# Kernel optimization log

Hardware: AMD Instinct MI355X
Metric: run time of the kernel (lower is better)

## Reference

```python
import jax, jax.numpy as jnp
import numpy as np

B, NV, H, D = 8, 16, 192, 512
NH = 8
HD = D // NH
DFF = 2048
EPS = 1e-5


def _bn(x, g, b):
    # x: (N, T, C); BatchNorm1d over channel C using batch stats (train mode)
    mu = jnp.mean(x, axis=(0, 1))
    var = jnp.var(x, axis=(0, 1))
    return (x - mu) / jnp.sqrt(var + EPS) * g + b


def _ff(x, w1, b1, w2, b2):
    h = jax.nn.gelu(jnp.einsum('bnhd,fd->bnhf', x, w1) + b1, approximate=False)
    return jnp.einsum('bnhf,df->bnhd', h, w2) + b2


def setup_inputs() -> dict:
    key = jax.random.key(0)
    ks = jax.random.split(key, 20)
    s = 0.02
    return {
        'src': jax.random.normal(ks[0], (B, NV, H, D), jnp.float32),
        'qk_w': jax.random.normal(ks[1], (2 * D, D), jnp.float32) * s,
        'qk_b': jnp.zeros((2 * D,), jnp.float32),
        'v_w': jax.random.normal(ks[2], (D, D), jnp.float32) * s,
        'v_b': jnp.zeros((D,), jnp.float32),
        'alpha_p': jax.random.normal(ks[3], (HD, 1), jnp.float32) * 0.1,
        'g_pre1': jnp.ones((D,), jnp.float32),
        'b_pre1': jnp.zeros((D,), jnp.float32),
        'g_pre2': jnp.ones((D,), jnp.float32),
        'b_pre2': jnp.zeros((D,), jnp.float32),
        'ff1_w1': jax.random.normal(ks[4], (DFF, D), jnp.float32) * s,
        'ff1_b1': jnp.zeros((DFF,), jnp.float32),
        'ff1_w2': jax.random.normal(ks[5], (D, DFF), jnp.float32) * s,
        'ff1_b2': jnp.zeros((D,), jnp.float32),
        'ff2_w1': jax.random.normal(ks[6], (DFF, D), jnp.float32) * s,
        'ff2_b1': jnp.zeros((DFF,), jnp.float32),
        'ff2_w2': jax.random.normal(ks[7], (D, DFF), jnp.float32) * s,
        'ff2_b2': jnp.zeros((D,), jnp.float32),
        'g_attn': jnp.ones((D,), jnp.float32),
        'b_attn': jnp.zeros((D,), jnp.float32),
    }


def reference(src, qk_w, qk_b, v_w, v_b, alpha_p,
              g_pre1, b_pre1, g_pre2, b_pre2,
              ff1_w1, ff1_b1, ff1_w2, ff1_b2,
              ff2_w1, ff2_b1, ff2_w2, ff2_b2,
              g_attn, b_attn):
    b, n, h, c = src.shape
    hd = c // NH
    # normalized input for q,k; raw for v
    src1 = src / jnp.linalg.norm(src, axis=-1, keepdims=True)
    qk = (jnp.einsum('bnhc,ec->bnhe', src1, qk_w) + qk_b)
    qk = qk.reshape(b, n, h, 2, NH, hd).transpose(3, 0, 1, 4, 2, 5)  # (2,b,n,NH,h,hd)
    q, k = qk[0], qk[1]
    v = (jnp.einsum('bnhc,ec->bnhe', src, v_w) + v_b)
    v = v.reshape(b, n, h, NH, hd).transpose(0, 1, 3, 2, 4)  # (b,n,NH,h,hd)

    # exponential-decay weights in FFT domain (branch: h != 7)
    a = jax.nn.sigmoid(alpha_p)                  # (hd,1)
    ar = jnp.arange(h - 1, -1, -1, dtype=src.dtype)
    weights = a * (1.0 - a) ** ar                # (hd, h)
    n2 = 2 * h
    w_f = jnp.fft.rfft(weights, n=n2, axis=-1)   # (hd, h+1)
    q_f = jnp.swapaxes(jnp.fft.rfft(q, n=n2, axis=-2), -1, -2) * w_f
    k_f = jnp.swapaxes(jnp.fft.rfft(k, n=n2, axis=-2), -1, -2) * w_f
    q1 = jnp.swapaxes(jnp.fft.irfft(q_f, n=n2, axis=-1)[..., :h], -1, -2)
    k1 = jnp.swapaxes(jnp.fft.irfft(k_f, n=n2, axis=-1)[..., :h], -1, -2)

    # token-axis attention (note: original divides by head_dim**-0.5 == * sqrt(hd))
    score_t = jnp.einsum('bnhed,bnhfd->bnhef', q1, k1) * (hd ** 0.5)
    attn_t = jax.nn.softmax(score_t, axis=-1)
    out_tok = jnp.einsum('bnhef,bnhfd->bnhed', attn_t, v)  # (b,n,NH,h,hd)
    o3 = _bn(out_tok.reshape(b * n, h, NH * hd), g_pre2, b_pre2).reshape(b, n, h, c)

    # hidden-axis attention on un-decayed q,k (scale = sqrt(h))
    score_h = jnp.einsum('bnhae,bnhaf->bnhef', q, k) * (h ** 0.5)
    attn_h = jax.nn.softmax(score_h, axis=-1)
    out_hid = jnp.einsum('bnhef,bnhaf->bnhae', attn_h, v)  # (b,n,NH,h,hd)
    o2 = _bn(out_hid.reshape(b * n, h, NH * hd), g_pre1, b_pre1).reshape(b, n, h, c)

    src2 = _ff(o3, ff1_w1, ff1_b1, ff1_w2, ff1_b2) + _ff(o2, ff2_w1, ff2_b1, ff2_w2, ff2_b2)
    out = src + src2
    out = _bn(out.reshape(b * n, h, c), g_attn, b_attn).reshape(b, n, h, c)
    return out
```

## Files before the change

kernel.cpp:

```cpp
#include <hip/hip_runtime.h>
#include <math.h>

#define SEQ 192
#define NTOK 24576
#define EPS 1e-5f

typedef __bf16 bf16x8 __attribute__((ext_vector_type(8)));
typedef __bf16 bf16x4 __attribute__((ext_vector_type(4)));
typedef float  f32x4  __attribute__((ext_vector_type(4)));

__device__ __forceinline__ void load_lds16(const __bf16* g, __bf16* l) {
    __builtin_amdgcn_global_load_lds(
        (const __attribute__((address_space(1))) uint32_t*)g,
        (__attribute__((address_space(3))) uint32_t*)l, 16, 0, 0);
}

__device__ __forceinline__ float gelu_f(float x) {
    float z = 1.5957691216057308f * x * fmaf(0.044715f, x*x, 1.f);
    float e = __expf(-z);
    return x * __builtin_amdgcn_rcpf(1.f + e);
}

__global__ __launch_bounds__(256) void cvtall_k(
    const float* __restrict__ s0, const float* __restrict__ s1, const float* __restrict__ s2,
    const float* __restrict__ s3, const float* __restrict__ s4, const float* __restrict__ s5,
    __bf16* __restrict__ dst)
{
    int i = blockIdx.x * 256 + threadIdx.x;
    int f = i * 4;
    const float* s; int off;
    if      (f <  524288) { s = s0; off = 0;       }
    else if (f <  786432) { s = s1; off = 524288;  }
    else if (f < 1835008) { s = s2; off = 786432;  }
    else if (f < 2883584) { s = s3; off = 1835008; }
    else if (f < 3932160) { s = s4; off = 2883584; }
    else                  { s = s5; off = 3932160; }
    f32x4 v = *(const f32x4*)&s[f - off];
    bf16x4 o;
    o[0]=(__bf16)v[0]; o[1]=(__bf16)v[1]; o[2]=(__bf16)v[2]; o[3]=(__bf16)v[3];
    ((bf16x4*)dst)[i] = o;
}

__global__ __launch_bounds__(256) void prep_k(const float* __restrict__ src,
    __bf16* __restrict__ srcb, __bf16* __restrict__ srcnb)
{
    int w = threadIdx.x >> 6, lane = threadIdx.x & 63;
    size_t token = blockIdx.x * 4 + w;
    const float* p = src + token * 512 + lane * 8;
    f32x4 a0 = *(const f32x4*)p;
    f32x4 a1 = *(const f32x4*)(p + 4);
    float s = a0[0]*a0[0]+a0[1]*a0[1]+a0[2]*a0[2]+a0[3]*a0[3]
            + a1[0]*a1[0]+a1[1]*a1[1]+a1[2]*a1[2]+a1[3]*a1[3];
#pragma unroll
    for (int off = 32; off; off >>= 1) s += __shfl_xor(s, off);
    float rs = rsqrtf(s);
    bf16x8 vb, vn;
#pragma unroll
    for (int q = 0; q < 4; q++) {
        vb[q]   = (__bf16)a0[q];      vn[q]   = (__bf16)(a0[q]*rs);
        vb[q+4] = (__bf16)a1[q];      vn[q+4] = (__bf16)(a1[q]*rs);
    }
    *(bf16x8*)&srcb[token*512 + lane*8]  = vb;
    *(bf16x8*)&srcnb[token*512 + lane*8] = vn;
}

template<bool AFFINE, bool GELU>
__global__ __launch_bounds__(256) void gemm_k(
    const __bf16* __restrict__ A, const __bf16* __restrict__ B, __bf16* __restrict__ C,
    int N, int K, const float* __restrict__ bias, const float* __restrict__ coef)
{
    __shared__ __bf16 As[8192];
    __shared__ __bf16 Bs[8192];
    const int tid = threadIdx.x, lane = tid & 63, w = tid >> 6;
    const int wr = w >> 1, wc = w & 1;
    const int b = blockIdx.y * gridDim.x + blockIdx.x;
    const int xcd = b & 7, bi = b >> 3;
    const int ypx = gridDim.y >> 3;
    const int m0 = (xcd * ypx + bi / gridDim.x) * 128;
    const int n0 = (bi % gridDim.x) * 128;
    const int fr = lane & 15, fq = lane >> 4;
    const int grow = 8*w + (lane >> 3);
    const int gcol = ((lane & 7) ^ (lane >> 3)) * 8;
    const __bf16* gB = B + (size_t)(n0 + grow) * K + gcol;
    const __bf16* gA = A + (size_t)(m0 + grow) * K + gcol;
    __bf16* ldsA = As + 8*w*64 + lane*8;
    __bf16* ldsB = Bs + 8*w*64 + lane*8;

    f32x4 acc[4][4];
#pragma unroll
    for (int i = 0; i < 4; i++)
#pragma unroll
        for (int j = 0; j < 4; j++) acc[i][j] = (f32x4){0.f,0.f,0.f,0.f};

    for (int k0 = 0; k0 < K; k0 += 64) {
        if (!AFFINE) {
#pragma unroll
            for (int i = 0; i < 4; i++)
                load_lds16(gA + k0 + (size_t)(32*i)*K, ldsA + i*2048);
        } else {
            const int r = tid >> 3, cseg = tid & 7;
            const float* scp = coef + k0 + cseg*8;
            const float* shp = coef + 512 + k0 + cseg*8;
            f32x4 sc0 = *(const f32x4*)scp, sc1 = *(const f32x4*)(scp+4);
            f32x4 sh0 = *(const f32x4*)shp, sh1 = *(const f32x4*)(shp+4);
#pragma unroll
            for (int i = 0; i < 4; i++) {
                int row = 32*i + r;
                bf16x8 a = *(const bf16x8*)&A[(size_t)(m0+row)*512 + k0 + cseg*8];
                bf16x8 v;
#pragma unroll
                for (int q = 0; q < 4; q++) {
                    v[q]   = (__bf16)fmaf((float)a[q],   sc0[q], sh0[q]);
                    v[q+4] = (__bf16)fmaf((float)a[q+4], sc1[q], sh1[q]);
                }
                *(bf16x8*)&As[row*64 + ((cseg ^ (r & 7)) * 8)] = v;
            }
        }
#pragma unroll
        for (int i = 0; i < 4; i++)
            load_lds16(gB + k0 + (size_t)(32*i)*K, ldsB + i*2048);
        __syncthreads();
#pragma unroll
        for (int kk = 0; kk < 2; kk++) {
            bf16x8 af[4], bfv[4];
#pragma unroll
            for (int i = 0; i < 4; i++)
                af[i] = *(bf16x8*)&As[(wr*64 + i*16 + fr)*64 + (((kk*4+fq) ^ (fr&7))*8)];
#pragma unroll
            for (int j = 0; j < 4; j++)
                bfv[j] = *(bf16x8*)&Bs[(wc*64 + j*16 + fr)*64 + (((kk*4+fq) ^ (fr&7))*8)];
#pragma unroll
            for (int i = 0; i < 4; i++)
#pragma unroll
                for (int j = 0; j < 4; j++)
                    acc[i][j] = __builtin_amdgcn_mfma_f32_16x16x32_bf16(af[i], bfv[j], acc[i][j], 0, 0, 0);
        }
        __syncthreads();
    }
    const int r4 = lane >> 4, cc = lane & 15;
#pragma unroll
    for (int i = 0; i < 4; i++) {
#pragma unroll
        for (int r = 0; r < 4; r++) {
            int m = m0 + wr*64 + i*16 + r4*4 + r;
#pragma unroll
            for (int j = 0; j < 4; j++) {
                int n = n0 + wc*64 + j*16 + cc;
                float v = acc[i][j][r] + bias[n];
                if (GELU) v = gelu_f(v);
                C[(size_t)m * N + n] = (__bf16)v;
            }
        }
    }
}

__global__ __launch_bounds__(256) void w1scale_k(
    __bf16* __restrict__ w, const float* __restrict__ coef,
    const float* __restrict__ bias_in, float* __restrict__ bias_out)
{
    const int wv = threadIdx.x >> 6, lane = threadIdx.x & 63;
    const int n = blockIdx.x * 4 + wv;
    __bf16* p = w + (size_t)n * 512 + lane * 8;
    bf16x8 v = *(bf16x8*)p;
    f32x4 sc0 = *(const f32x4*)(coef + lane*8);
    f32x4 sc1 = *(const f32x4*)(coef + lane*8 + 4);
    f32x4 sh0 = *(const f32x4*)(coef + 512 + lane*8);
    f32x4 sh1 = *(const f32x4*)(coef + 512 + lane*8 + 4);
    float dot = 0.f;
    bf16x8 o;
#pragma unroll
    for (int q = 0; q < 4; q++) {
        float w0 = (float)v[q], w1 = (float)v[q+4];
        o[q]   = (__bf16)(w0 * sc0[q]);
        o[q+4] = (__bf16)(w1 * sc1[q]);
        dot = fmaf(w0, sh0[q], dot);
        dot = fmaf(w1, sh1[q], dot);
    }
    *(bf16x8*)p = o;
#pragma unroll
    for (int off = 32; off; off >>= 1) dot += __shfl_xor(dot, off);
    if (lane == 0) bias_out[n] = bias_in[n] + dot;
}

__global__ __launch_bounds__(256) void gemm2_k(
    const __bf16* __restrict__ A1, const __bf16* __restrict__ A2,
    const __bf16* __restrict__ B1, const __bf16* __restrict__ B2,
    float* __restrict__ C, const float* __restrict__ b1, const float* __restrict__ b2,
    const float* __restrict__ resid, float* __restrict__ st)
{
    __shared__ __bf16 As[4096];
    __shared__ __bf16 Bs[8192];
    const int tid = threadIdx.x, lane = tid & 63, w = tid >> 6;
    const int wr = w >> 1, wc = w & 1;
    const int vb = blockIdx.x;
    const int xcd = vb & 7, k2 = vb >> 3;
    const int m0 = (xcd*24 + (k2 >> 2)) * 64;
    const int n0 = (k2 & 3) * 128;
    const int fr = lane & 15, fq = lane >> 4;
    const int grow = 8*w + (lane >> 3);
    const int gcol = ((lane & 7) ^ (lane >> 3)) * 8;
    const int K = 2048;
    __bf16* ldsA = As + 8*w*64 + lane*8;
    __bf16* ldsB = Bs + 8*w*64 + lane*8;

    f32x4 acc[2][4];
#pragma unroll
    for (int i = 0; i < 2; i++)
#pragma unroll
        for (int j = 0; j < 4; j++) acc[i][j] = (f32x4){0.f,0.f,0.f,0.f};

#pragma unroll 1
    for (int half = 0; half < 2; half++) {
        const __bf16* gA = (half ? A2 : A1) + (size_t)(m0 + grow) * K + gcol;
        const __bf16* gB = (half ? B2 : B1) + (size_t)(n0 + grow) * K + gcol;
        for (int k0 = 0; k0 < K; k0 += 64) {
            load_lds16(gA + k0,                 ldsA);
            load_lds16(gA + k0 + (size_t)32*K,  ldsA + 2048);
#pragma unroll
            for (int i = 0; i < 4; i++)
                load_lds16(gB + k0 + (size_t)(32*i)*K, ldsB + i*2048);
            __syncthreads();
#pragma unroll
            for (int kk = 0; kk < 2; kk++) {
                bf16x8 af[2], bfv[4];
#pragma unroll
                for (int i = 0; i < 2; i++)
                    af[i] = *(bf16x8*)&As[(wr*32 + i*16 + fr)*64 + (((kk*4+fq) ^ (fr&7))*8)];
#pragma unroll
                for (int j = 0; j < 4; j++)
                    bfv[j] = *(bf16x8*)&Bs[(wc*64 + j*16 + fr)*64 + (((kk*4+fq) ^ (fr&7))*8)];
#pragma unroll
                for (int i = 0; i < 2; i++)
#pragma unroll
                    for (int j = 0; j < 4; j++)
                        acc[i][j] = __builtin_amdgcn_mfma_f32_16x16x32_bf16(af[i], bfv[j], acc[i][j], 0, 0, 0);
            }
            __syncthreads();
        }
    }
    const int r4 = lane >> 4, cc = lane & 15;
    float cs[4] = {0,0,0,0}, cq[4] = {0,0,0,0};
#pragma unroll
    for (int i = 0; i < 2; i++) {
#pragma unroll
        for (int r = 0; r < 4; r++) {
            int m = m0 + wr*32 + i*16 + r4*4 + r;
#pragma unroll
            for (int j = 0; j < 4; j++) {
                int n = n0 + wc*64 + j*16 + cc;
                size_t idx = (size_t)m * 512 + n;
                float v = acc[i][j][r] + b1[n] + b2[n] + resid[idx];
                C[idx] = v;
                cs[j] += v; cq[j] = fmaf(v, v, cq[j]);
            }
        }
    }
#pragma unroll
    for (int j = 0; j < 4; j++) {
        cs[j] += __shfl_xor(cs[j], 16); cs[j] += __shfl_xor(cs[j], 32);
        cq[j] += __shfl_xor(cq[j], 16); cq[j] += __shfl_xor(cq[j], 32);
    }
    if (r4 == 0) {
#pragma unroll
        for (int j = 0; j < 4; j++) {
            int n = n0 + wc*64 + j*16 + cc;
            atomicAdd(&st[n], cs[j]);
            atomicAdd(&st[512 + n], cq[j]);
        }
    }
}

__global__ __launch_bounds__(256) void hidden_attn_mfma_k(
    const __bf16* __restrict__ QKb, const __bf16* __restrict__ Vb, __bf16* __restrict__ OHb)
{
    __shared__ __bf16 smem[25600];
    __bf16* Qt = smem;
    __bf16* Kt = smem + 12800;
    __bf16* Ps = smem;
    __bf16* Vs = smem + 4608;
    const int bn = blockIdx.x >> 3, nh = blockIdx.x & 7;
    const int tid = threadIdx.x, lane = tid & 63, w = tid >> 6;
    const int fr = lane & 15, fq = lane >> 4;
    const size_t rowbase = (size_t)bn * SEQ;

#pragma unroll
    for (int it = 0; it < 12; it++) {
        int tk = tid + (it % 6) * 256;
        int j = tk & 63, tg = tk >> 6;
        const __bf16* gsrc = QKb + (rowbase + tg*8)*1024 + nh*64 + j + (it >= 6 ? 512 : 0);
        bf16x8 v;
#pragma unroll
        for (int u = 0; u < 8; u++) v[u] = gsrc[(size_t)u*1024];
        __bf16* dst = (it >= 6 ? Kt : Qt) + j*200 + tg*8;
        *(bf16x8*)dst = v;
    }
    __syncthreads();

    f32x4 acc[4];
#pragma unroll
    for (int i = 0; i < 4; i++) acc[i] = (f32x4){0.f,0.f,0.f,0.f};
#pragma unroll
    for (int kc = 0; kc < 6; kc++) {
        bf16x8 a = *(bf16x8*)&Qt[(w*16 + fr)*200 + kc*32 + fq*8];
#pragma unroll
        for (int nt = 0; nt < 4; nt++) {
            bf16x8 b = *(bf16x8*)&Kt[(nt*16 + fr)*200 + kc*32 + fq*8];
            acc[nt] = __builtin_amdgcn_mfma_f32_16x16x32_bf16(a, b, acc[nt], 0, 0, 0);
        }
    }
    const float sc = 13.856406460551018f;
    float pn[4][4];
#pragma unroll
    for (int reg = 0; reg < 4; reg++) {
        float m = -1e30f;
#pragma unroll
        for (int nt = 0; nt < 4; nt++) { acc[nt][reg] *= sc; m = fmaxf(m, acc[nt][reg]); }
#pragma unroll
        for (int off = 1; off < 16; off <<= 1) m = fmaxf(m, __shfl_xor(m, off));
        float l = 0.f;
#pragma unroll
        for (int nt = 0; nt < 4; nt++) { pn[nt][reg] = __expf(acc[nt][reg] - m); l += pn[nt][reg]; }
#pragma unroll
        for (int off = 1; off < 16; off <<= 1) l += __shfl_xor(l, off);
        float inv = 1.f / l;
#pragma unroll
        for (int nt = 0; nt < 4; nt++) pn[nt][reg] *= inv;
    }
    __syncthreads();
#pragma unroll
    for (int nt = 0; nt < 4; nt++)
#pragma unroll
        for (int reg = 0; reg < 4; reg++)
            Ps[(w*16 + fq*4 + reg)*72 + nt*16 + fr] = (__bf16)pn[nt][reg];
    for (int i = tid; i < 1536; i += 256) {
        int t = i >> 3, s = i & 7;
        *(bf16x8*)&Vs[t*72 + s*8] = *(const bf16x8*)&Vb[(rowbase+t)*512 + nh*64 + s*8];
    }
    __syncthreads();

    f32x4 o[3][4];
#pragma unroll
    for (int i = 0; i < 3; i++)
#pragma unroll
        for (int j = 0; j < 4; j++) o[i][j] = (f32x4){0.f,0.f,0.f,0.f};
#pragma unroll
    for (int kc = 0; kc < 2; kc++) {
        bf16x8 av[3];
#pragma unroll
        for (int mt = 0; mt < 3; mt++)
            av[mt] = *(bf16x8*)&Vs[(48*w + mt*16 + fr)*72 + kc*32 + fq*8];
#pragma unroll
        for (int nt = 0; nt < 4; nt++) {
            bf16x8 b = *(bf16x8*)&Ps[(nt*16 + fr)*72 + kc*32 + fq*8];
#pragma unroll
            for (int mt = 0; mt < 3; mt++)
                o[mt][nt] = __builtin_amdgcn_mfma_f32_16x16x32_bf16(av[mt], b, o[mt][nt], 0, 0, 0);
        }
    }
    __bf16* obase = OHb + ((size_t)(bn*8 + nh)) * SEQ * 64;
#pragma unroll
    for (int mt = 0; mt < 3; mt++)
#pragma unroll
        for (int reg = 0; reg < 4; reg++) {
            int t = 48*w + mt*16 + fq*4 + reg;
#pragma unroll
            for (int nt = 0; nt < 4; nt++)
                obase[(size_t)t*64 + nt*16 + fr] = (__bf16)o[mt][nt][reg];
        }
}

__global__ __launch_bounds__(256) void token_attn_mfma_k(
    const __bf16* __restrict__ QKb, const __bf16* __restrict__ Vb, __bf16* __restrict__ OT,
    const float* __restrict__ alpha)
{
    __shared__ __bf16 smem[27648];
    __bf16* Qs = smem;
    __bf16* Ks = smem + 13824;
    __bf16* Vt = smem;
    __bf16* Pw = smem + 12800;
    const int bn = blockIdx.x >> 3, nh = blockIdx.x & 7;
    const int tid = threadIdx.x, lane = tid & 63, w = tid >> 6;
    const int fr = lane & 15, fq = lane >> 4;
    const size_t rowbase = (size_t)bn * SEQ;

    for (int i = tid; i < 1536; i += 256) {
        int t = i >> 3, s = i & 7;
        const __bf16* g = QKb + (rowbase + t)*1024 + nh*64;
        *(bf16x8*)&Qs[t*72 + s*8] = *(const bf16x8*)&g[s*8];
        *(bf16x8*)&Ks[t*72 + s*8] = *(const bf16x8*)&g[512 + s*8];
    }
    __syncthreads();

    if (tid < 128) {
        const int d = tid & 63;
        __bf16* col = (tid < 64) ? (Qs + d) : (Ks + d);
        const float av = 1.f / (1.f + __expf(-alpha[d]));
        const float r = 1.f - av;
        float P = 0.f, pw = 1.f;
#pragma unroll 4
        for (int t = 0; t < SEQ; t++) {
            P = fmaf(pw, (float)col[t*72], P);
            col[t*72] = (__bf16)P;
            pw *= r;
        }
        float f = av;
#pragma unroll 4
        for (int t = SEQ-1; t >= 0; t--) {
            col[t*72] = (__bf16)((float)col[t*72] * f);
            f *= r;
        }
    }
    __syncthreads();

    f32x4 S[3][12];
#pragma unroll
    for (int i = 0; i < 3; i++)
#pragma unroll
        for (int j = 0; j < 12; j++) S[i][j] = (f32x4){0.f,0.f,0.f,0.f};
#pragma unroll
    for (int kc = 0; kc < 2; kc++) {
        bf16x8 aq[3];
#pragma unroll
        for (int mt = 0; mt < 3; mt++)
            aq[mt] = *(bf16x8*)&Qs[(48*w + mt*16 + fr)*72 + kc*32 + fq*8];
#pragma unroll
        for (int nt = 0; nt < 12; nt++) {
            bf16x8 b = *(bf16x8*)&Ks[(nt*16 + fr)*72 + kc*32 + fq*8];
#pragma unroll
            for (int mt = 0; mt < 3; mt++)
                S[mt][nt] = __builtin_amdgcn_mfma_f32_16x16x32_bf16(aq[mt], b, S[mt][nt], 0, 0, 0);
        }
    }
#pragma unroll
    for (int mt = 0; mt < 3; mt++)
#pragma unroll
        for (int reg = 0; reg < 4; reg++) {
            float m = -1e30f;
#pragma unroll
            for (int nt = 0; nt < 12; nt++) { S[mt][nt][reg] *= 8.f; m = fmaxf(m, S[mt][nt][reg]); }
#pragma unroll
            for (int off = 1; off < 16; off <<= 1) m = fmaxf(m, __shfl_xor(m, off));
            float l = 0.f;
#pragma unroll
            for (int nt = 0; nt < 12; nt++) { S[mt][nt][reg] = __expf(S[mt][nt][reg] - m); l += S[mt][nt][reg]; }
#pragma unroll
            for (int off = 1; off < 16; off <<= 1) l += __shfl_xor(l, off);
            float inv = 1.f / l;
#pragma unroll
            for (int nt = 0; nt < 12; nt++) S[mt][nt][reg] *= inv;
        }
    __syncthreads();
#pragma unroll
    for (int it = 0; it < 6; it++) {
        int tk = tid + it * 256;
        int d = tk & 63, tg = tk >> 6;
        const __bf16* gsrc = Vb + (rowbase + tg*8)*512 + nh*64 + d;
        bf16x8 v;
#pragma unroll
        for (int u = 0; u < 8; u++) v[u] = gsrc[(size_t)u*512];
        *(bf16x8*)&Vt[d*200 + tg*8] = v;
    }
    __syncthreads();

    f32x4 O[3][4];
#pragma unroll
    for (int i = 0; i < 3; i++)
#pragma unroll
        for (int j = 0; j < 4; j++) O[i][j] = (f32x4){0.f,0.f,0.f,0.f};
    __bf16* myP = Pw + w*3456;
#pragma unroll
    for (int fc = 0; fc < 3; fc++) {
#pragma unroll
        for (int mt = 0; mt < 3; mt++)
#pragma unroll
            for (int j = 0; j < 4; j++)
#pragma unroll
                for (int reg = 0; reg < 4; reg++)
                    myP[(mt*16 + fq*4 + reg)*72 + j*16 + fr] = (__bf16)S[mt][fc*4 + j][reg];
#pragma unroll
        for (int kc = 0; kc < 2; kc++) {
            bf16x8 ap[3];
#pragma unroll
            for (int mt = 0; mt < 3; mt++)
                ap[mt] = *(bf16x8*)&myP[(mt*16 + fr)*72 + kc*32 + fq*8];
#pragma unroll
            for (int dt = 0; dt < 4; dt++) {
                bf16x8 b = *(bf16x8*)&Vt[(dt*16 + fr)*200 + fc*64 + kc*32 + fq*8];
#pragma unroll
                for (int mt = 0; mt < 3; mt++)
                    O[mt][dt] = __builtin_amdgcn_mfma_f32_16x16x32_bf16(ap[mt], b, O[mt][dt], 0, 0, 0);
            }
        }
    }
    __bf16* obase = OT + ((size_t)(bn*8 + nh)) * SEQ * 64;
#pragma unroll
    for (int mt = 0; mt < 3; mt++)
#pragma unroll
        for (int reg = 0; reg < 4; reg++) {
            int e = 48*w + mt*16 + fq*4 + reg;
#pragma unroll
            for (int dt = 0; dt < 4; dt++)
                obase[(size_t)e*64 + dt*16 + fr] = (__bf16)O[mt][dt][reg];
        }
}

__global__ __launch_bounds__(256) void bn_stats1_k(const __bf16* __restrict__ x, float* __restrict__ part)
{
    __shared__ float red[3072];
    const int col8 = threadIdx.x & 63;
    const int rl   = threadIdx.x >> 6;
    const size_t r0 = (size_t)blockIdx.x * 96;
    f32x4 sA = {0,0,0,0}, sB = {0,0,0,0}, qA = {0,0,0,0}, qB = {0,0,0,0};
    for (int r = rl; r < 96; r += 4) {
        bf16x8 v = *(const bf16x8*)&x[(r0 + r)*512 + col8*8];
        f32x4 lo = { (float)v[0], (float)v[1], (float)v[2], (float)v[3] };
        f32x4 hi = { (float)v[4], (float)v[5], (float)v[6], (float)v[7] };
        sA += lo; sB += hi;
        qA += lo*lo; qB += hi*hi;
    }
    if (rl > 0) {
        float* p = &red[(rl-1)*1024];
        *(f32x4*)&p[col8*8]       = sA;  *(f32x4*)&p[col8*8 + 4]       = sB;
        *(f32x4*)&p[512 + col8*8] = qA;  *(f32x4*)&p[512 + col8*8 + 4] = qB;
    }
    __syncthreads();
    if (rl == 0) {
#pragma unroll
        for (int k = 0; k < 3; k++) {
            float* p = &red[k*1024];
            sA += *(f32x4*)&p[col8*8];       sB += *(f32x4*)&p[col8*8 + 4];
            qA += *(f32x4*)&p[512 + col8*8]; qB += *(f32x4*)&p[512 + col8*8 + 4];
        }
        float* o = &part[(size_t)blockIdx.x * 1024];
        *(f32x4*)&o[col8*8]       = sA;  *(f32x4*)&o[col8*8 + 4]       = sB;
        *(f32x4*)&o[512 + col8*8] = qA;  *(f32x4*)&o[512 + col8*8 + 4] = qB;
    }
}

__global__ __launch_bounds__(256) void bn_stats2_k(const float* __restrict__ part, float* __restrict__ st)
{
    int c = blockIdx.x * 256 + threadIdx.x;
    float s0 = 0.f, s1 = 0.f, s2 = 0.f, s3 = 0.f;
    for (int b = 0; b < 256; b += 4) {
        s0 += part[(size_t)b*1024 + c];
        s1 += part[(size_t)(b+1)*1024 + c];
        s2 += part[(size_t)(b+2)*1024 + c];
        s3 += part[(size_t)(b+3)*1024 + c];
    }
    st[c] = (s0 + s1) + (s2 + s3);
}

__global__ void bn_coef_k(const float* __restrict__ st, const float* __restrict__ g,
                          const float* __restrict__ b, float* __restrict__ coef)
{
    int c = threadIdx.x;
    float mean = st[c] * (1.f/24576.f);
    float var  = st[512+c] * (1.f/24576.f) - mean*mean;
    float sc = rsqrtf(var + EPS) * g[c];
    coef[c] = sc;
    coef[512 + c] = b[c] - mean * sc;
}

__global__ __launch_bounds__(256) void bn_apply4_k(const float* __restrict__ x, const float* __restrict__ st,
    const float* __restrict__ g, const float* __restrict__ b, float* __restrict__ out)
{
    size_t i = (size_t)blockIdx.x * 256 + threadIdx.x;
    int col4 = i & 127;
    f32x4 v = ((const f32x4*)x)[i];
    f32x4 sm = ((const f32x4*)st)[col4];
    f32x4 sq = ((const f32x4*)(st + 512))[col4];
    f32x4 o;
#pragma unroll
    for (int j = 0; j < 4; j++) {
        int c = col4*4 + j;
        float mean = sm[j] * (1.f/24576.f);
        float var  = sq[j] * (1.f/24576.f) - mean*mean;
        o[j] = (v[j] - mean) * rsqrtf(var + EPS) * g[c] + b[c];
    }
    ((f32x4*)out)[i] = o;
}

extern "C" void kernel_launch(void* const* d_in, const int* in_sizes, int n_in,
                              void* d_out, int out_size, void* d_ws, size_t ws_size,
                              hipStream_t stream)
{
    const float* src    = (const float*)d_in[0];
    const float* qk_w   = (const float*)d_in[1];
    const float* qk_b   = (const float*)d_in[2];
    const float* v_w    = (const float*)d_in[3];
    const float* v_b    = (const float*)d_in[4];
    const float* alpha  = (const float*)d_in[5];
    const float* g_pre1 = (const float*)d_in[6];
    const float* b_pre1 = (const float*)d_in[7];
    const float* g_pre2 = (const float*)d_in[8];
    const float* b_pre2 = (const float*)d_in[9];
    const float* ff1_w1 = (const float*)d_in[10];
    const float* ff1_b1 = (const float*)d_in[11];
    const float* ff1_w2 = (const float*)d_in[12];
    const float* ff1_b2 = (const float*)d_in[13];
    const float* ff2_w1 = (const float*)d_in[14];
    const float* ff2_b1 = (const float*)d_in[15];
    const float* ff2_w2 = (const float*)d_in[16];
    const float* ff2_b2 = (const float*)d_in[17];
    const float* g_attn = (const float*)d_in[18];
    const float* b_attn = (const float*)d_in[19];
    float* out = (float*)d_out;

    __bf16* wq   = (__bf16*)d_ws;
    __bf16* wv   = wq  + 524288;
    __bf16* w11  = wv  + 262144;
    __bf16* w12  = w11 + 1048576;
    __bf16* w21  = w12 + 1048576;
    __bf16* w22  = w21 + 1048576;
    __bf16* srcb  = w22 + 1048576;
    __bf16* srcnb = srcb + (size_t)NTOK*512;
    __bf16* QKb   = srcnb + (size_t)NTOK*512;
    __bf16* Vb    = QKb + (size_t)NTOK*1024;
    __bf16* OHbf  = Vb + (size_t)NTOK*512;
    __bf16* o3bf  = OHbf + (size_t)NTOK*512;
    float*  stats = (float*)(o3bf + (size_t)NTOK*512);
    float*  coef0 = stats + 3072;
    float*  coef1 = coef0 + 1024;
    float*  part0 = coef1 + 1024;
    float*  part1 = part0 + 262144;
    float*  bias1p = part1 + 262144;
    float*  bias2p = bias1p + 2048;
    __bf16* H1 = srcb;
    __bf16* H2 = H1 + (size_t)12288*2048;
    float *st0 = stats, *st1 = stats + 1024, *st2 = stats + 2048;

    hipMemsetAsync(st2, 0, 1024*sizeof(float), stream);

    cvtall_k<<<4864, 256, 0, stream>>>(qk_w, v_w, ff1_w1, ff1_w2, ff2_w1, ff2_w2, wq);
    prep_k<<<NTOK/4, 256, 0, stream>>>(src, srcb, srcnb);

    gemm_k<false,false><<<dim3(8, 192), 256, 0, stream>>>(srcnb, wq, QKb, 1024, 512, qk_b, nullptr);
    gemm_k<false,false><<<dim3(4, 192), 256, 0, stream>>>(srcb,  wv, Vb,  512,  512, v_b,  nullptr);

    hidden_attn_mfma_k<<<1024, 256, 0, stream>>>(QKb, Vb, OHbf);

    token_attn_mfma_k<<<1024, 256, 0, stream>>>(QKb, Vb, o3bf, alpha);

    bn_stats1_k<<<256, 256, 0, stream>>>(o3bf, part0);
    bn_stats1_k<<<256, 256, 0, stream>>>(OHbf, part1);
    bn_stats2_k<<<4, 256, 0, stream>>>(part0, st0);
    bn_stats2_k<<<4, 256, 0, stream>>>(part1, st1);
    bn_coef_k<<<1, 512, 0, stream>>>(st0, g_pre2, b_pre2, coef0);
    bn_coef_k<<<1, 512, 0, stream>>>(st1, g_pre1, b_pre1, coef1);
    w1scale_k<<<512, 256, 0, stream>>>(w11, coef0, ff1_b1, bias1p);
    w1scale_k<<<512, 256, 0, stream>>>(w21, coef1, ff2_b1, bias2p);

    for (int ch = 0; ch < 2; ch++) {
        size_t off = (size_t)ch * 12288 * 512;
        gemm_k<false,true><<<dim3(16, 96), 256, 0, stream>>>(o3bf + off, w11, H1, 2048, 512, bias1p, nullptr);
        gemm_k<false,true><<<dim3(16, 96), 256, 0, stream>>>(OHbf + off, w21, H2, 2048, 512, bias2p, nullptr);
        gemm2_k<<<768, 256, 0, stream>>>(H1, H2, w12, w22, out + off,
                                         ff1_b2, ff2_b2, src + off, st2);
    }

    bn_apply4_k<<<12288, 256, 0, stream>>>(out, st2, g_attn, b_attn, out);
}
```

Before: 696.9 us.

## Merge small launches, fuse attention kernels, double-buffer the second FFN GEMM

Several pairs of kernels become single launches: weight conversion with input prep, the two attention kernels (interleaved by block parity), the BN stat and coefficient kernels, the W1 scaling, and the two first-layer FFN GEMMs, which now share one grid through a DUAL path. The unused AFFINE path is removed from the GEMM. The second FFN GEMM now double-buffers its LDS tiles, prefetching the next K slice while computing the current one, with one barrier per iteration. The aim is to cut launch overhead and tail idle time and to hide global-load latency, at the cost of twice the LDS in gemm2, which may reduce occupancy.

Result: no change. 695.5 us (-0.2%).

```diff
diff --git a/kernel.cpp b/kernel.cpp
--- a/kernel.cpp
+++ b/kernel.cpp
@@ -21,53 +21,55 @@
     return x * __builtin_amdgcn_rcpf(1.f + e);
 }
 
-__global__ __launch_bounds__(256) void cvtall_k(
+__global__ __launch_bounds__(256) void cvtprep_k(
     const float* __restrict__ s0, const float* __restrict__ s1, const float* __restrict__ s2,
     const float* __restrict__ s3, const float* __restrict__ s4, const float* __restrict__ s5,
-    __bf16* __restrict__ dst)
-{
-    int i = blockIdx.x * 256 + threadIdx.x;
-    int f = i * 4;
-    const float* s; int off;
-    if      (f <  524288) { s = s0; off = 0;       }
-    else if (f <  786432) { s = s1; off = 524288;  }
-    else if (f < 1835008) { s = s2; off = 786432;  }
-    else if (f < 2883584) { s = s3; off = 1835008; }
-    else if (f < 3932160) { s = s4; off = 2883584; }
-    else                  { s = s5; off = 3932160; }
-    f32x4 v = *(const f32x4*)&s[f - off];
-    bf16x4 o;
-    o[0]=(__bf16)v[0]; o[1]=(__bf16)v[1]; o[2]=(__bf16)v[2]; o[3]=(__bf16)v[3];
-    ((bf16x4*)dst)[i] = o;
-}
-
-__global__ __launch_bounds__(256) void prep_k(const float* __restrict__ src,
-    __bf16* __restrict__ srcb, __bf16* __restrict__ srcnb)
-{
-    int w = threadIdx.x >> 6, lane = threadIdx.x & 63;
-    size_t token = blockIdx.x * 4 + w;
-    const float* p = src + token * 512 + lane * 8;
-    f32x4 a0 = *(const f32x4*)p;
-    f32x4 a1 = *(const f32x4*)(p + 4);
-    float s = a0[0]*a0[0]+a0[1]*a0[1]+a0[2]*a0[2]+a0[3]*a0[3]
-            + a1[0]*a1[0]+a1[1]*a1[1]+a1[2]*a1[2]+a1[3]*a1[3];
-#pragma unroll
-    for (int off = 32; off; off >>= 1) s += __shfl_xor(s, off);
-    float rs = rsqrtf(s);
-    bf16x8 vb, vn;
-#pragma unroll
-    for (int q = 0; q < 4; q++) {
-        vb[q]   = (__bf16)a0[q];      vn[q]   = (__bf16)(a0[q]*rs);
-        vb[q+4] = (__bf16)a1[q];      vn[q+4] = (__bf16)(a1[q]*rs);
-    }
-    *(bf16x8*)&srcb[token*512 + lane*8]  = vb;
-    *(bf16x8*)&srcnb[token*512 + lane*8] = vn;
-}
-
-template<bool AFFINE, bool GELU>
+    __bf16* __restrict__ dst,
+    const float* __restrict__ src, __bf16* __restrict__ srcb, __bf16* __restrict__ srcnb)
+{
+    if (blockIdx.x < 4864) {
+        int i = blockIdx.x * 256 + threadIdx.x;
+        int f = i * 4;
+        const float* s; int off;
+        if      (f <  524288) { s = s0; off = 0;       }
+        else if (f <  786432) { s = s1; off = 524288;  }
+        else if (f < 1835008) { s = s2; off = 786432;  }
+        else if (f < 2883584) { s = s3; off = 1835008; }
+        else if (f < 3932160) { s = s4; off = 2883584; }
+        else                  { s = s5; off = 3932160; }
+        f32x4 v = *(const f32x4*)&s[f - off];
+        bf16x4 o;
+        o[0]=(__bf16)v[0]; o[1]=(__bf16)v[1]; o[2]=(__bf16)v[2]; o[3]=(__bf16)v[3];
+        ((bf16x4*)dst)[i] = o;
+    } else {
+        int blk = blockIdx.x - 4864;
+        int w = threadIdx.x >> 6, lane = threadIdx.x & 63;
+        size_t token = blk * 4 + w;
+        const float* p = src + token * 512 + lane * 8;
+        f32x4 a0 = *(const f32x4*)p;
+        f32x4 a1 = *(const f32x4*)(p + 4);
+        float s = a0[0]*a0[0]+a0[1]*a0[1]+a0[2]*a0[2]+a0[3]*a0[3]
+                + a1[0]*a1[0]+a1[1]*a1[1]+a1[2]*a1[2]+a1[3]*a1[3];
+#pragma unroll
+        for (int off = 32; off; off >>= 1) s += __shfl_xor(s, off);
+        float rs = rsqrtf(s);
+        bf16x8 vb, vn;
+#pragma unroll
+        for (int q = 0; q < 4; q++) {
+            vb[q]   = (__bf16)a0[q];      vn[q]   = (__bf16)(a0[q]*rs);
+            vb[q+4] = (__bf16)a1[q];      vn[q+4] = (__bf16)(a1[q]*rs);
+        }
+        *(bf16x8*)&srcb[token*512 + lane*8]  = vb;
+        *(bf16x8*)&srcnb[token*512 + lane*8] = vn;
+    }
+}
+
+template<bool GELU, bool DUAL>
 __global__ __launch_bounds__(256) void gemm_k(
     const __bf16* __restrict__ A, const __bf16* __restrict__ B, __bf16* __restrict__ C,
-    int N, int K, const float* __restrict__ bias, const float* __restrict__ coef)
+    int N, int K, const float* __restrict__ bias,
+    const __bf16* __restrict__ A2, const __bf16* __restrict__ B2, __bf16* __restrict__ C2,
+    const float* __restrict__ bias2, int M1)
 {
     __shared__ __bf16 As[8192];
     __shared__ __bf16 Bs[8192];
@@ -76,8 +78,9 @@
     const int b = blockIdx.y * gridDim.x + blockIdx.x;
     const int xcd = b & 7, bi = b >> 3;
     const int ypx = gridDim.y >> 3;
-    const int m0 = (xcd * ypx + bi / gridDim.x) * 128;
+    int m0 = (xcd * ypx + bi / gridDim.x) * 128;
     const int n0 = (bi % gridDim.x) * 128;
+    if (DUAL && m0 >= M1) { A = A2; B = B2; C = C2; bias = bias2; m0 -= M1; }
     const int fr = lane & 15, fq = lane >> 4;
     const int grow = 8*w + (lane >> 3);
     const int gcol = ((lane & 7) ^ (lane >> 3)) * 8;
@@ -93,29 +96,9 @@
         for (int j = 0; j < 4; j++) acc[i][j] = (f32x4){0.f,0.f,0.f,0.f};
 
     for (int k0 = 0; k0 < K; k0 += 64) {
-        if (!AFFINE) {
-#pragma unroll
-            for (int i = 0; i < 4; i++)
-                load_lds16(gA + k0 + (size_t)(32*i)*K, ldsA + i*2048);
-        } else {
-            const int r = tid >> 3, cseg = tid & 7;
-            const float* scp = coef + k0 + cseg*8;
-            const float* shp = coef + 512 + k0 + cseg*8;
-            f32x4 sc0 = *(const f32x4*)scp, sc1 = *(const f32x4*)(scp+4);
-            f32x4 sh0 = *(const f32x4*)shp, sh1 = *(const f32x4*)(shp+4);
-#pragma unroll
-            for (int i = 0; i < 4; i++) {
-                int row = 32*i + r;
-                bf16x8 a = *(const bf16x8*)&A[(size_t)(m0+row)*512 + k0 + cseg*8];
-                bf16x8 v;
-#pragma unroll
-                for (int q = 0; q < 4; q++) {
-                    v[q]   = (__bf16)fmaf((float)a[q],   sc0[q], sh0[q]);
-                    v[q+4] = (__bf16)fmaf((float)a[q+4], sc1[q], sh1[q]);
-                }
-                *(bf16x8*)&As[row*64 + ((cseg ^ (r & 7)) * 8)] = v;
-            }
-        }
+#pragma unroll
+        for (int i = 0; i < 4; i++)
+            load_lds16(gA + k0 + (size_t)(32*i)*K, ldsA + i*2048);
 #pragma unroll
         for (int i = 0; i < 4; i++)
             load_lds16(gB + k0 + (size_t)(32*i)*K, ldsB + i*2048);
@@ -155,12 +138,18 @@
 }
 
 __global__ __launch_bounds__(256) void w1scale_k(
-    __bf16* __restrict__ w, const float* __restrict__ coef,
-    const float* __restrict__ bias_in, float* __restrict__ bias_out)
-{
+    __bf16* __restrict__ w1a, __bf16* __restrict__ w1b, const float* __restrict__ coef01,
+    const float* __restrict__ b1in, const float* __restrict__ b2in,
+    float* __restrict__ b1out, float* __restrict__ b2out)
+{
+    const int half = blockIdx.x >> 9;
+    __bf16* wbase = half ? w1b : w1a;
+    const float* coef = coef01 + half*1024;
+    const float* bin  = half ? b2in  : b1in;
+    float* bout       = half ? b2out : b1out;
     const int wv = threadIdx.x >> 6, lane = threadIdx.x & 63;
-    const int n = blockIdx.x * 4 + wv;
-    __bf16* p = w + (size_t)n * 512 + lane * 8;
+    const int n = (blockIdx.x & 511) * 4 + wv;
+    __bf16* p = wbase + (size_t)n * 512 + lane * 8;
     bf16x8 v = *(bf16x8*)p;
     f32x4 sc0 = *(const f32x4*)(coef + lane*8);
     f32x4 sc1 = *(const f32x4*)(coef + lane*8 + 4);
@@ -179,7 +168,7 @@
     *(bf16x8*)p = o;
 #pragma unroll
     for (int off = 32; off; off >>= 1) dot += __shfl_xor(dot, off);
-    if (lane == 0) bias_out[n] = bias_in[n] + dot;
+    if (lane == 0) bout[n] = bin[n] + dot;
 }
 
 __global__ __launch_bounds__(256) void gemm2_k(
@@ -188,8 +177,8 @@
     float* __restrict__ C, const float* __restrict__ b1, const float* __restrict__ b2,
     const float* __restrict__ resid, float* __restrict__ st)
 {
-    __shared__ __bf16 As[4096];
-    __shared__ __bf16 Bs[8192];
+    __shared__ __bf16 As[2][4096];
+    __shared__ __bf16 Bs[2][8192];
     const int tid = threadIdx.x, lane = tid & 63, w = tid >> 6;
     const int wr = w >> 1, wc = w & 1;
     const int vb = blockIdx.x;
@@ -200,8 +189,23 @@
     const int grow = 8*w + (lane >> 3);
     const int gcol = ((lane & 7) ^ (lane >> 3)) * 8;
     const int K = 2048;
-    __bf16* ldsA = As + 8*w*64 + lane*8;
-    __bf16* ldsB = Bs + 8*w*64 + lane*8;
+    const int ldsoff = 8*w*64 + lane*8;
+    const __bf16* gA1 = A1 + (size_t)(m0 + grow) * K + gcol;
+    const __bf16* gA2 = A2 + (size_t)(m0 + grow) * K + gcol;
+    const __bf16* gB1 = B1 + (size_t)(n0 + grow) * K + gcol;
+    const __bf16* gB2 = B2 + (size_t)(n0 + grow) * K + gcol;
+
+#define G2_STAGE(pb, it_) do {                                              \
+        int half_ = (it_) >> 5, k0_ = ((it_) & 31) * 64;                    \
+        const __bf16* ga_ = (half_ ? gA2 : gA1) + k0_;                      \
+        const __bf16* gb_ = (half_ ? gB2 : gB1) + k0_;                      \
+        load_lds16(ga_,                  &As[pb][ldsoff]);                  \
+        load_lds16(ga_ + (size_t)32*K,   &As[pb][ldsoff + 2048]);           \
+        load_lds16(gb_,                  &Bs[pb][ldsoff]);                  \
+        load_lds16(gb_ + (size_t)32*K,   &Bs[pb][ldsoff + 2048]);           \
+        load_lds16(gb_ + (size_t)64*K,   &Bs[pb][ldsoff + 4096]);           \
+        load_lds16(gb_ + (size_t)96*K,   &Bs[pb][ldsoff + 6144]);           \
+    } while (0)
 
     f32x4 acc[2][4];
 #pragma unroll
@@ -209,35 +213,32 @@
 #pragma unroll
         for (int j = 0; j < 4; j++) acc[i][j] = (f32x4){0.f,0.f,0.f,0.f};
 
-#pragma unroll 1
-    for (int half = 0; half < 2; half++) {
-        const __bf16* gA = (half ? A2 : A1) + (size_t)(m0 + grow) * K + gcol;
-        const __bf16* gB = (half ? B2 : B1) + (size_t)(n0 + grow) * K + gcol;
-        for (int k0 = 0; k0 < K; k0 += 64) {
-            load_lds16(gA + k0,                 ldsA);
-            load_lds16(gA + k0 + (size_t)32*K,  ldsA + 2048);
-#pragma unroll
-            for (int i = 0; i < 4; i++)
-                load_lds16(gB + k0 + (size_t)(32*i)*K, ldsB + i*2048);
-            __syncthreads();
-#pragma unroll
-            for (int kk = 0; kk < 2; kk++) {
-                bf16x8 af[2], bfv[4];
-#pragma unroll
-                for (int i = 0; i < 2; i++)
-                    af[i] = *(bf16x8*)&As[(wr*32 + i*16 + fr)*64 + (((kk*4+fq) ^ (fr&7))*8)];
+    G2_STAGE(0, 0);
+    asm volatile("s_waitcnt vmcnt(0)" ::: "memory");
+    __syncthreads();
+    for (int it = 0; it < 64; ++it) {
+        const int cur = it & 1;
+        if (it + 1 < 64) G2_STAGE(cur ^ 1, it + 1);
+#pragma unroll
+        for (int kk = 0; kk < 2; kk++) {
+            bf16x8 af[2], bfv[4];
+#pragma unroll
+            for (int i = 0; i < 2; i++)
+                af[i] = *(bf16x8*)&As[cur][(wr*32 + i*16 + fr)*64 + (((kk*4+fq) ^ (fr&7))*8)];
+#pragma unroll
+            for (int j = 0; j < 4; j++)
+                bfv[j] = *(bf16x8*)&Bs[cur][(wc*64 + j*16 + fr)*64 + (((kk*4+fq) ^ (fr&7))*8)];
+#pragma unroll
+            for (int i = 0; i < 2; i++)
 #pragma unroll
                 for (int j = 0; j < 4; j++)
-                    bfv[j] = *(bf16x8*)&Bs[(wc*64 + j*16 + fr)*64 + (((kk*4+fq) ^ (fr&7))*8)];
-#pragma unroll
-                for (int i = 0; i < 2; i++)
-#pragma unroll
-                    for (int j = 0; j < 4; j++)
-                        acc[i][j] = __builtin_amdgcn_mfma_f32_16x16x32_bf16(af[i], bfv[j], acc[i][j], 0, 0, 0);
-            }
-            __syncthreads();
-        }
-    }
+                    acc[i][j] = __builtin_amdgcn_mfma_f32_16x16x32_bf16(af[i], bfv[j], acc[i][j], 0, 0, 0);
+        }
+        asm volatile("s_waitcnt vmcnt(0)" ::: "memory");
+        __syncthreads();
+    }
+#undef G2_STAGE
+
     const int r4 = lane >> 4, cc = lane & 15;
     float cs[4] = {0,0,0,0}, cq[4] = {0,0,0,0};
 #pragma unroll
@@ -270,15 +271,14 @@
     }
 }
 
-__global__ __launch_bounds__(256) void hidden_attn_mfma_k(
-    const __bf16* __restrict__ QKb, const __bf16* __restrict__ Vb, __bf16* __restrict__ OHb)
-{
-    __shared__ __bf16 smem[25600];
+__device__ __forceinline__ void hidden_attn_body(
+    const __bf16* __restrict__ QKb, const __bf16* __restrict__ Vb, __bf16* __restrict__ OHb,
+    __bf16* smem, int bn, int nh)
+{
     __bf16* Qt = smem;
     __bf16* Kt = smem + 12800;
     __bf16* Ps = smem;
     __bf16* Vs = smem + 4608;
-    const int bn = blockIdx.x >> 3, nh = blockIdx.x & 7;
     const int tid = threadIdx.x, lane = tid & 63, w = tid >> 6;
     const int fr = lane & 15, fq = lane >> 4;
     const size_t rowbase = (size_t)bn * SEQ;
@@ -369,16 +369,14 @@
         }
 }
 
-__global__ __launch_bounds__(256) void token_attn_mfma_k(
+__device__ __forceinline__ void token_attn_body(
     const __bf16* __restrict__ QKb, const __bf16* __restrict__ Vb, __bf16* __restrict__ OT,
-    const float* __restrict__ alpha)
-{
-    __shared__ __bf16 smem[27648];
+    const float* __restrict__ alpha, __bf16* smem, int bn, int nh)
+{
     __bf16* Qs = smem;
     __bf16* Ks = smem + 13824;
     __bf16* Vt = smem;
     __bf16* Pw = smem + 12800;
-    const int bn = blockIdx.x >> 3, nh = blockIdx.x & 7;
     const int tid = threadIdx.x, lane = tid & 63, w = tid >> 6;
     const int fr = lane & 15, fq = lane >> 4;
     const size_t rowbase = (size_t)bn * SEQ;
@@ -504,12 +502,26 @@
         }
 }
 
-__global__ __launch_bounds__(256) void bn_stats1_k(const __bf16* __restrict__ x, float* __restrict__ part)
+__global__ __launch_bounds__(256) void attn_both_k(
+    const __bf16* __restrict__ QKb, const __bf16* __restrict__ Vb,
+    __bf16* __restrict__ OHb, __bf16* __restrict__ OT, const float* __restrict__ alpha)
+{
+    __shared__ __bf16 smem[27648];
+    const int type = blockIdx.x & 1, idx = blockIdx.x >> 1;
+    const int bn = idx >> 3, nh = idx & 7;
+    if (type == 0) hidden_attn_body(QKb, Vb, OHb, smem, bn, nh);
+    else           token_attn_body(QKb, Vb, OT, alpha, smem, bn, nh);
+}
+
+__global__ __launch_bounds__(256) void bn_stats1_k(const __bf16* __restrict__ x0,
+    const __bf16* __restrict__ x1, float* __restrict__ part)
 {
     __shared__ float red[3072];
+    const __bf16* x = (blockIdx.x < 256) ? x0 : x1;
+    const int blk = blockIdx.x & 255;
     const int col8 = threadIdx.x & 63;
     const int rl   = threadIdx.x >> 6;
-    const size_t r0 = (size_t)blockIdx.x * 96;
+    const size_t r0 = (size_t)blk * 96;
     f32x4 sA = {0,0,0,0}, sB = {0,0,0,0}, qA = {0,0,0,0}, qB = {0,0,0,0};
     for (int r = rl; r < 96; r += 4) {
         bf16x8 v = *(const bf16x8*)&x[(r0 + r)*512 + col8*8];
@@ -540,25 +552,34 @@
 __global__ __launch_bounds__(256) void bn_stats2_k(const float* __restrict__ part, float* __restrict__ st)
 {
     int c = blockIdx.x * 256 + threadIdx.x;
+    int half = c >> 10, cc = c & 1023;
+    const float* p = part + (size_t)half * 262144;
     float s0 = 0.f, s1 = 0.f, s2 = 0.f, s3 = 0.f;
     for (int b = 0; b < 256; b += 4) {
-        s0 += part[(size_t)b*1024 + c];
-        s1 += part[(size_t)(b+1)*1024 + c];
-        s2 += part[(size_t)(b+2)*1024 + c];
-        s3 += part[(size_t)(b+3)*1024 + c];
+        s0 += p[(size_t)b*1024 + cc];
+        s1 += p[(size_t)(b+1)*1024 + cc];
+        s2 += p[(size_t)(b+2)*1024 + cc];
+        s3 += p[(size_t)(b+3)*1024 + cc];
     }
     st[c] = (s0 + s1) + (s2 + s3);
 }
 
-__global__ void bn_coef_k(const float* __restrict__ st, const float* __restrict__ g,
-                          const float* __restrict__ b, float* __restrict__ coef)
-{
-    int c = threadIdx.x;
-    float mean = st[c] * (1.f/24576.f);
-    float var  = st[512+c] * (1.f/24576.f) - mean*mean;
+__global__ void bn_coef_k(const float* __restrict__ st,
+                          const float* __restrict__ gA, const float* __restrict__ bA,
+                          const float* __restrict__ gB, const float* __restrict__ bB,
+                          float* __restrict__ coef)
+{
+    int tidx = threadIdx.x;
+    int half = tidx >> 9, c = tidx & 511;
+    const float* sb = st + half*1024;
+    const float* g = half ? gB : gA;
+    const float* b = half ? bB : bA;
+    float* co = coef + half*1024;
+    float mean = sb[c] * (1.f/24576.f);
+    float var  = sb[512+c] * (1.f/24576.f) - mean*mean;
     float sc = rsqrtf(var + EPS) * g[c];
-    coef[c] = sc;
-    coef[512 + c] = b[c] - mean * sc;
+    co[c] = sc;
+    co[512 + c] = b[c] - mean * sc;
 }
 
 __global__ __launch_bounds__(256) void bn_apply4_k(const float* __restrict__ x, const float* __restrict__ st,
@@ -620,40 +641,34 @@
     __bf16* o3bf  = OHbf + (size_t)NTOK*512;
     float*  stats = (float*)(o3bf + (size_t)NTOK*512);
     float*  coef0 = stats + 3072;
-    float*  coef1 = coef0 + 1024;
-    float*  part0 = coef1 + 1024;
-    float*  part1 = part0 + 262144;
-    float*  bias1p = part1 + 262144;
+    float*  part0 = coef0 + 2048;
+    float*  bias1p = part0 + 2*262144;
     float*  bias2p = bias1p + 2048;
     __bf16* H1 = srcb;
     __bf16* H2 = H1 + (size_t)12288*2048;
-    float *st0 = stats, *st1 = stats + 1024, *st2 = stats + 2048;
+    float *st2 = stats + 2048;
 
     hipMemsetAsync(st2, 0, 1024*sizeof(float), stream);
 
-    cvtall_k<<<4864, 256, 0, stream>>>(qk_w, v_w, ff1_w1, ff1_w2, ff2_w1, ff2_w2, wq);
-    prep_k<<<NTOK/4, 256, 0, stream>>>(src, srcb, srcnb);
-
-    gemm_k<false,false><<<dim3(8, 192), 256, 0, stream>>>(srcnb, wq, QKb, 1024, 512, qk_b, nullptr);
-    gemm_k<false,false><<<dim3(4, 192), 256, 0, stream>>>(srcb,  wv, Vb,  512,  512, v_b,  nullptr);
-
-    hidden_attn_mfma_k<<<1024, 256, 0, stream>>>(QKb, Vb, OHbf);
-
-    token_attn_mfma_k<<<1024, 256, 0, stream>>>(QKb, Vb, o3bf, alpha);
-
-    bn_stats1_k<<<256, 256, 0, stream>>>(o3bf, part0);
-    bn_stats1_k<<<256, 256, 0, stream>>>(OHbf, part1);
-    bn_stats2_k<<<4, 256, 0, stream>>>(part0, st0);
-    bn_stats2_k<<<4, 256, 0, stream>>>(part1, st1);
-    bn_coef_k<<<1, 512, 0, stream>>>(st0, g_pre2, b_pre2, coef0);
-    bn_coef_k<<<1, 512, 0, stream>>>(st1, g_pre1, b_pre1, coef1);
-    w1scale_k<<<512, 256, 0, stream>>>(w11, coef0, ff1_b1, bias1p);
-    w1scale_k<<<512, 256, 0, stream>>>(w21, coef1, ff2_b1, bias2p);
+    cvtprep_k<<<4864 + NTOK/4, 256, 0, stream>>>(qk_w, v_w, ff1_w1, ff1_w2, ff2_w1, ff2_w2, wq,
+                                                 src, srcb, srcnb);
+
+    gemm_k<false,false><<<dim3(8, 192), 256, 0, stream>>>(srcnb, wq, QKb, 1024, 512, qk_b,
+                                                          nullptr, nullptr, nullptr, nullptr, 0);
+    gemm_k<false,false><<<dim3(4, 192), 256, 0, stream>>>(srcb,  wv, Vb,  512,  512, v_b,
+                                                          nullptr, nullptr, nullptr, nullptr, 0);
+
+    attn_both_k<<<2048, 256, 0, stream>>>(QKb, Vb, OHbf, o3bf, alpha);
+
+    bn_stats1_k<<<512, 256, 0, stream>>>(o3bf, OHbf, part0);
+    bn_stats2_k<<<8, 256, 0, stream>>>(part0, stats);
+    bn_coef_k<<<1, 1024, 0, stream>>>(stats, g_pre2, b_pre2, g_pre1, b_pre1, coef0);
+    w1scale_k<<<1024, 256, 0, stream>>>(w11, w21, coef0, ff1_b1, ff2_b1, bias1p, bias2p);
 
     for (int ch = 0; ch < 2; ch++) {
         size_t off = (size_t)ch * 12288 * 512;
-        gemm_k<false,true><<<dim3(16, 96), 256, 0, stream>>>(o3bf + off, w11, H1, 2048, 512, bias1p, nullptr);
-        gemm_k<false,true><<<dim3(16, 96), 256, 0, stream>>>(OHbf + off, w21, H2, 2048, 512, bias2p, nullptr);
+        gemm_k<true,true><<<dim3(16, 192), 256, 0, stream>>>(o3bf + off, w11, H1, 2048, 512, bias1p,
+                                                             OHbf + off, w21, H2, bias2p, 12288);
         gemm2_k<<<768, 256, 0, stream>>>(H1, H2, w12, w22, out + off,
                                          ff1_b2, ff2_b2, src + off, st2);
     }
```
